# Kernel tuning notes

Hardware: AMD Instinct MI355X
Metric: run time of the kernel (lower is better)

## Reference

```python
import jax, jax.numpy as jnp
import numpy as np

# 1x1 Conv2d == channel contraction
def _conv(x, w):
    return jnp.einsum('bctn,oc->botn', x, w)

# BatchNorm2d in eval mode; p rows = (gamma, beta, running_mean, running_var)
def _bn(x, p, eps=1e-5):
    g, b, m, v = p
    s = g * jax.lax.rsqrt(v + eps)
    return x * s[None, :, None, None] + (b - m * s)[None, :, None, None]


def _forward(x, pos_2d, w_pos, b_pos, w_expand, bn_expand, w1, bn1, w2, bn2,
             w_ag, bn_ag, w_ag_s, b_ag_s, w_att, bn_att, w_att_s, b_att_s, W):
    B, T, J, Cp, N = x.shape
    C = J * Cp
    # rearrange 'b t j c n -> b (j c) t n'
    f = x.transpose(0, 2, 3, 1, 4).reshape(B, C, T, N)
    # pairwise expansion: h[b,:,t,i,j] = concat(f[b,:,t,i], f[b,:,t,j])  -> (B,2C,T,N*N)
    x1 = jnp.broadcast_to(f[:, :, :, :, None], (B, C, T, N, N))
    x2 = jnp.broadcast_to(f[:, :, :, None, :], (B, C, T, N, N))
    h = jnp.concatenate([x1, x2], axis=1).reshape(B, 2 * C, T, N * N)
    # relative 2D position embedding (first 2 coord channels)
    p = pos_2d[:, :, :, :2, :].transpose(0, 2, 3, 1, 4).reshape(B, 2 * J, T, N)
    rel = (p[:, :, :, :, None] - p[:, :, :, None, :]).reshape(B, 2 * J, T, N * N)
    pos_emb = _conv(rel, w_pos) + b_pos[None, :, None, None]
    # VAL trunk (dropout = identity in eval)
    h = jax.nn.relu(_bn(_conv(h, w_expand), bn_expand)) + pos_emb
    res = h
    h = jax.nn.relu(_bn(_conv(h, w1), bn1))
    h = jax.nn.relu(_bn(_conv(h, w2), bn2))
    h = res + h
    ag = _conv(jax.nn.relu(_bn(_conv(h, w_ag), bn_ag)), w_ag_s) + b_ag_s[None, :, None, None]
    ag = ag.reshape(B, -1, T, N, N)          # (B,Co,T,N,N)
    att = _conv(jax.nn.relu(_bn(_conv(h, w_att), bn_att)), w_att_s) + b_att_s[None, :, None, None]
    att = att.reshape(B, 1, T, N, N)
    # self / transfer terms, broadcast over receiver axis i
    f_self = jnp.einsum('bctn,cd->bdtn', f, W[0])[:, :, :, None, :]  # (B,Co,T,1,N)
    f_tran = jnp.einsum('bctn,cd->bdtn', f, W[1])[:, :, :, None, :] * ag
    E = jnp.eye(N, dtype=f.dtype)[None, None, None]                  # (1,1,1,N,N)
    f_conv = E * f_self + (1.0 - E) * f_tran
    att = jax.nn.softmax(att, axis=-1)
    f_fuse = jnp.sum(f_conv * att, axis=-1) + f                      # (B,Co,T,N)
    return f_fuse.reshape(B, J, Cp, T, N).transpose(0, 3, 1, 2, 4)   # (B,T,J,Cp,N)


def setup_inputs() -> dict:
    key = jax.random.key(0)
    ks = iter(jax.random.split(key, 64))
    B, T, J, Cp, N = 8, 128, 17, 32, 4
    C = J * Cp            # 544
    Cin = 2 * C           # 1088 (VAL in_channels)
    Co = C                # 544 (out_channels)

    def w(shape, s=0.03):
        return jax.random.normal(next(ks), shape, jnp.float32) * s

    def bn(c):
        return jnp.stack([
            1.0 + 0.1 * jax.random.normal(next(ks), (c,), jnp.float32),
            0.1 * jax.random.normal(next(ks), (c,), jnp.float32),
            0.1 * jax.random.normal(next(ks), (c,), jnp.float32),
            0.5 + jax.random.uniform(next(ks), (c,), jnp.float32),
        ])

    return dict(
        x=jax.random.normal(next(ks), (B, T, J, Cp, N), jnp.float32),
        pos_2d=jax.random.normal(next(ks), (B, T, J, 2, N), jnp.float32),
        w_pos=w((Cin, 2 * J)), b_pos=w((Cin,)),
        w_expand=w((Cin, Cin)), bn_expand=bn(Cin),
        w1=w((Cin, Cin)), bn1=bn(Cin),
        w2=w((Cin, Cin)), bn2=bn(Cin),
        w_ag=w((Cin, Cin)), bn_ag=bn(Cin),
        w_ag_s=w((Co, Cin)), b_ag_s=w((Co,)),
        w_att=w((Cin, Cin)), bn_att=bn(Cin),
        w_att_s=w((1, Cin)), b_att_s=w((1,)),
        W=w((2, Co, Co), 0.05),
    )


def reference(x, pos_2d, w_pos, b_pos, w_expand, bn_expand, w1, bn1, w2, bn2,
              w_ag, bn_ag, w_ag_s, b_ag_s, w_att, bn_att, w_att_s, b_att_s, W):
    return _forward(x, pos_2d, w_pos, b_pos, w_expand, bn_expand, w1, bn1, w2, bn2,
                    w_ag, bn_ag, w_ag_s, b_ag_s, w_att, bn_att, w_att_s, b_att_s, W)
```

## Files before the change

kernel.cpp:

```cpp
#include <hip/hip_runtime.h>

typedef unsigned short u16;
typedef unsigned int   u32;
typedef __attribute__((ext_vector_type(4))) float f32x4;
typedef __attribute__((ext_vector_type(8))) short short8;

#define DI static __device__ __forceinline__

DI u16 f2bf(float x){ union{float f;u32 u;}v; v.f=x; u32 r=v.u + 0x7fffu + ((v.u>>16)&1u); return (u16)(r>>16); }
DI float bf2f(u16 h){ union{u32 u;float f;}v; v.u=((u32)h)<<16; return v.f; }

DI void gl_lds16(const u16* g, u16* l){
  __builtin_amdgcn_global_load_lds((const __attribute__((address_space(1))) void*)g,
                                   (__attribute__((address_space(3))) void*)l, 16, 0, 0);
}


__global__ void k_bnprep(const float* __restrict__ bnE, const float* __restrict__ bn1,
                         const float* __restrict__ bn2, const float* __restrict__ bnA,
                         const float* __restrict__ bnT, float* __restrict__ out){
  int i = blockIdx.x*256 + threadIdx.x;
  if(i >= 5*1088) return;
  int w = i/1088, c = i - w*1088;
  const float* b = (w==0)?bnE:(w==1)?bn1:(w==2)?bn2:(w==3)?bnA:bnT;
  float g=b[c], be=b[1088+c], mu=b[2176+c], va=b[3264+c];
  float s = g / sqrtf(va + 1e-5f);
  out[w*2176 + c] = s;
  out[w*2176 + 1088 + c] = be - mu*s;
}

__global__ void k_zero(float* p, int n){ int i = blockIdx.x*256+threadIdx.x; if(i<n) p[i]=0.f; }

__global__ void k_pack_f(const float* __restrict__ x, float* __restrict__ fmat,
                         u16* __restrict__ fhi, u16* __restrict__ flo){
  int bt = blockIdx.x;
  const float* xr = x + (size_t)bt*2176;
  for(int t=threadIdx.x; t<2176; t+=256){
    int c = t>>2, n = t&3;
    float v = xr[t];
    size_t o = (size_t)(bt*4+n)*544 + c;
    fmat[o] = v;
    u16 h = f2bf(v); fhi[o]=h; flo[o]=f2bf(v - bf2f(h));
  }
}

__global__ void k_pack_w(const float* __restrict__ src, int off1, int off2, int O1,
                         int rs, int cs, int O, int K,
                         u16* __restrict__ dhi, u16* __restrict__ dlo){
  int o = blockIdx.y;
  int k = blockIdx.x*256 + threadIdx.x;
  if(k >= K) return;
  float v = 0.f;
  if(o < O){
    size_t idx = (o<O1) ? (size_t)off1 + (size_t)o*rs + (size_t)k*cs
                        : (size_t)off2 + (size_t)(o-O1)*rs + (size_t)k*cs;
    v = src[idx];
  }
  size_t d = (size_t)o*K + k;
  u16 h=f2bf(v); dhi[d]=h; dlo[d]=f2bf(v - bf2f(h));
}

__global__ void k_q(const float* __restrict__ pos, const float* __restrict__ w_pos,
                    float* __restrict__ q){
  int m = blockIdx.x; int bt = m>>2, n = m&3;
  __shared__ float pr[34];
  if(threadIdx.x<34){ int j = threadIdx.x>>1, d = threadIdx.x&1;
    pr[threadIdx.x] = pos[(size_t)bt*136 + j*8 + d*4 + n]; }
  __syncthreads();
  for(int o=threadIdx.x;o<1088;o+=256){
    const float* wr = w_pos + (size_t)o*34;
    float s = 0.f;
    #pragma unroll
    for(int k=0;k<34;k++) s += pr[k]*wr[k];
    q[(size_t)m*1088 + o] = s;
  }
}

__global__ void k_expand(const float* __restrict__ uv, const float* __restrict__ q,
                         const float* __restrict__ bn, const float* __restrict__ b_pos,
                         u16* __restrict__ hh, u16* __restrict__ hl){
  __shared__ float su[4][1088], sv[4][1088], sq[4][1088];
  int bt = blockIdx.x;
  for(int t=threadIdx.x; t<4*1088; t+=256){
    int r = t/1088, o = t - r*1088;
    su[r][o] = uv[(size_t)(bt*4+r)*2176 + o];
    sv[r][o] = uv[(size_t)(bt*4+r)*2176 + 1088 + o];
    sq[r][o] = q[(size_t)(bt*4+r)*1088 + o];
  }
  __syncthreads();
  for(int t=threadIdx.x; t<16*1088; t+=256){
    int ij = t/1088, o = t - ij*1088; int i = ij>>2, j = ij&3;
    float xv = bn[o]*(su[i][o]+sv[j][o]) + bn[1088+o];
    xv = fmaxf(xv,0.f) + sq[i][o]-sq[j][o]+b_pos[o];
    size_t idx = (size_t)(bt*16+ij)*1088 + o;
    u16 h=f2bf(xv); hh[idx]=h; hl[idx]=f2bf(xv-bf2f(h));
  }
}

template<int EPI>
__global__ __launch_bounds__(256,2)
void k_gemm(const u16* __restrict__ Ahi, const u16* __restrict__ Alo,
            const u16* __restrict__ Bhi, const u16* __restrict__ Blo,
            int K, int Nout, int ldo,
            float* __restrict__ out_f, u16* __restrict__ out_hi, u16* __restrict__ out_lo,
            const float* __restrict__ sv, const float* __restrict__ tv,
            const u16* __restrict__ res_hi, const u16* __restrict__ res_lo,
            const float* __restrict__ bias,
            const float* __restrict__ wred, float* __restrict__ red_out)
{
  __shared__ u16 Ah[2][4096], Al[2][4096], Bh[2][4096], Bl[2][4096];
  __shared__ float red[128];
  const int tid = threadIdx.x, lane = tid&63, wave = tid>>6;
  const int wm = wave>>1, wn = wave&1;

  const int gx = gridDim.x, gy = gridDim.y;
  const int flat = blockIdx.y*gx + blockIdx.x;
  const int chunk = (gx*gy) >> 3;
  const int p = (flat & 7)*chunk + (flat >> 3);
  const int bx = p/gy, by = p - bx*gy;
  const int m0 = bx*128, n0 = by*128;
  if(EPI==4 && tid<128) red[tid]=0.f;

  auto stage = [&](int buf, int kt){
    const int k0 = kt*32;
    #pragma unroll
    for(int c=0;c<2;c++){
      int s   = (wave*2+c)*64 + lane;
      int row = s>>2;
      int kg  = (s&3) ^ ((row>>1)&3);
      size_t ga = (size_t)(m0+row)*K + k0 + kg*8;
      size_t gb = (size_t)(n0+row)*K + k0 + kg*8;
      int lo = (wave*2+c)*512;
      gl_lds16(Ahi+ga, &Ah[buf][lo]);
      gl_lds16(Alo+ga, &Al[buf][lo]);
      gl_lds16(Bhi+gb, &Bh[buf][lo]);
      gl_lds16(Blo+gb, &Bl[buf][lo]);
    }
  };

  f32x4 acc[4][4];
  #pragma unroll
  for(int i=0;i<4;i++)
    #pragma unroll
    for(int j=0;j<4;j++){ acc[i][j][0]=0.f; acc[i][j][1]=0.f; acc[i][j][2]=0.f; acc[i][j][3]=0.f; }

  const int NT = K>>5;
  stage(0,0);
  stage(1,1);
  asm volatile("s_waitcnt vmcnt(8)" ::: "memory");
  __builtin_amdgcn_sched_barrier(0);
  __builtin_amdgcn_s_barrier();

  const int swz = ((lane>>4) ^ (((lane&15)>>1)&3))<<3;
  const int iA = ((wm*64 + (lane&15))<<5) + swz;
  const int iB = ((wn*64 + (lane&15))<<5) + swz;

  for(int kt=0; kt<NT; ++kt){
    const int buf = kt&1;
    short8 ah[4],al[4],bh[4],bl[4];
    #pragma unroll
    for(int i=0;i<4;i++){
      ah[i] = *(const short8*)&Ah[buf][iA + i*512];
      al[i] = *(const short8*)&Al[buf][iA + i*512];
      bh[i] = *(const short8*)&Bh[buf][iB + i*512];
      bl[i] = *(const short8*)&Bl[buf][iB + i*512];
    }
    asm volatile("s_waitcnt lgkmcnt(0)" ::: "memory");
    __builtin_amdgcn_sched_barrier(0);
    __builtin_amdgcn_s_barrier();
    int kt2 = kt+2; if(kt2 > NT-1) kt2 = NT-1;
    stage(buf, kt2);
    __builtin_amdgcn_s_setprio(1);
    #pragma unroll
    for(int mi=0;mi<4;mi++)
      #pragma unroll
      for(int ni=0;ni<4;ni++)
        acc[mi][ni] = __builtin_amdgcn_mfma_f32_16x16x32_bf16(ah[mi],bh[ni],acc[mi][ni],0,0,0);
    #pragma unroll
    for(int mi=0;mi<4;mi++)
      #pragma unroll
      for(int ni=0;ni<4;ni++)
        acc[mi][ni] = __builtin_amdgcn_mfma_f32_16x16x32_bf16(al[mi],bh[ni],acc[mi][ni],0,0,0);
    #pragma unroll
    for(int mi=0;mi<4;mi++)
      #pragma unroll
      for(int ni=0;ni<4;ni++)
        acc[mi][ni] = __builtin_amdgcn_mfma_f32_16x16x32_bf16(ah[mi],bl[ni],acc[mi][ni],0,0,0);
    __builtin_amdgcn_s_setprio(0);
    asm volatile("s_waitcnt vmcnt(8)" ::: "memory");
    __builtin_amdgcn_sched_barrier(0);
    __builtin_amdgcn_s_barrier();
  }

  const int r0 = m0 + wm*64 + ((lane>>4)<<2);
  const int c0 = n0 + wn*64 + (lane&15);

  if constexpr (EPI==0){
    #pragma unroll
    for(int mi=0;mi<4;mi++)
      #pragma unroll
      for(int ni=0;ni<4;ni++){
        int col = c0 + ni*16;
        if(col < Nout){
          #pragma unroll
          for(int r=0;r<4;r++)
            out_f[(size_t)(r0+mi*16+r)*ldo + col] = acc[mi][ni][r];
        }
      }
  } else if constexpr (EPI==1 || EPI==2){
    #pragma unroll
    for(int mi=0;mi<4;mi++)
      #pragma unroll
      for(int ni=0;ni<4;ni++){
        int col = c0 + ni*16;
        if(col < Nout){
          float sc = sv[col], tc = tv[col];
          #pragma unroll
          for(int r=0;r<4;r++){
            float y = fmaxf(acc[mi][ni][r]*sc + tc, 0.f);
            size_t idx = (size_t)(r0+mi*16+r)*ldo + col;
            if(EPI==2) y += bf2f(res_hi[idx]) + bf2f(res_lo[idx]);
            u16 h = f2bf(y); out_hi[idx]=h; out_lo[idx]=f2bf(y - bf2f(h));
          }
        }
      }
  } else if constexpr (EPI==3){
    #pragma unroll
    for(int mi=0;mi<4;mi++)
      #pragma unroll
      for(int ni=0;ni<4;ni++){
        int col = c0 + ni*16;
        if(col < Nout){
          float bc = bias[col];
          #pragma unroll
          for(int r=0;r<4;r++)
            out_f[(size_t)(r0+mi*16+r)*ldo + col] = acc[mi][ni][r] + bc;
        }
      }
  } else {
    float rs4[4][4];
    #pragma unroll
    for(int mi=0;mi<4;mi++)
      #pragma unroll
      for(int r=0;r<4;r++) rs4[mi][r]=0.f;
    #pragma unroll
    for(int mi=0;mi<4;mi++)
      #pragma unroll
      for(int ni=0;ni<4;ni++){
        int col = c0 + ni*16;
        if(col < Nout){
          float sc = sv[col], tc = tv[col], wc = wred[col];
          #pragma unroll
          for(int r=0;r<4;r++)
            rs4[mi][r] += fmaxf(acc[mi][ni][r]*sc + tc, 0.f)*wc;
        }
      }
    #pragma unroll
    for(int off=1; off<16; off<<=1)
      #pragma unroll
      for(int mi=0;mi<4;mi++)
        #pragma unroll
        for(int r=0;r<4;r++)
          rs4[mi][r] += __shfl_xor(rs4[mi][r], off, 64);
    if((lane&15)==0){
      #pragma unroll
      for(int mi=0;mi<4;mi++)
        #pragma unroll
        for(int r=0;r<4;r++)
          atomicAdd(&red[wm*64 + mi*16 + ((lane>>4)<<2) + r], rs4[mi][r]);
    }
    __syncthreads();
    if(tid<128) atomicAdd(&red_out[m0+tid], red[tid]);
  }
}

__global__ void k_fuse(const float* __restrict__ logits, const float* __restrict__ ag,
                       const float* __restrict__ fsft, const float* __restrict__ fmat,
                       float* __restrict__ out){
  int bt = blockIdx.x;
  float a[4][4];
  #pragma unroll
  for(int i=0;i<4;i++){
    float l0=logits[bt*16+i*4+0], l1=logits[bt*16+i*4+1],
          l2=logits[bt*16+i*4+2], l3=logits[bt*16+i*4+3];
    float mx = fmaxf(fmaxf(l0,l1),fmaxf(l2,l3));
    float e0=__expf(l0-mx), e1=__expf(l1-mx), e2=__expf(l2-mx), e3=__expf(l3-mx);
    float inv = 1.f/(e0+e1+e2+e3);
    a[i][0]=e0*inv; a[i][1]=e1*inv; a[i][2]=e2*inv; a[i][3]=e3*inv;
  }
  for(int d=threadIdx.x; d<544; d+=256){
    float fsv[4], ftv[4], fv[4];
    #pragma unroll
    for(int j=0;j<4;j++){
      fsv[j] = fsft[(size_t)(bt*4+j)*1088 + d];
      ftv[j] = fsft[(size_t)(bt*4+j)*1088 + 544 + d];
      fv[j]  = fmat[(size_t)(bt*4+j)*544 + d];
    }
    float o4[4];
    #pragma unroll
    for(int i=0;i<4;i++){
      float s = fv[i];
      #pragma unroll
      for(int j=0;j<4;j++){
        float fc = (j==i) ? fsv[j] : ftv[j]*ag[(size_t)(bt*16+i*4+j)*544 + d];
        s += a[i][j]*fc;
      }
      o4[i]=s;
    }
    *(float4*)(out + ((size_t)bt*544 + d)*4) = make_float4(o4[0],o4[1],o4[2],o4[3]);
  }
}

extern "C" void kernel_launch(void* const* d_in, const int* in_sizes, int n_in,
                              void* d_out, int out_size, void* d_ws, size_t ws_size,
                              hipStream_t stream){
  (void)in_sizes; (void)n_in; (void)out_size; (void)ws_size;
  const float* x      = (const float*)d_in[0];
  const float* pos2d  = (const float*)d_in[1];
  const float* w_pos  = (const float*)d_in[2];
  const float* b_pos  = (const float*)d_in[3];
  const float* w_exp  = (const float*)d_in[4];
  const float* bnE    = (const float*)d_in[5];
  const float* w1     = (const float*)d_in[6];
  const float* bn1    = (const float*)d_in[7];
  const float* w2     = (const float*)d_in[8];
  const float* bn2    = (const float*)d_in[9];
  const float* w_ag   = (const float*)d_in[10];
  const float* bnA    = (const float*)d_in[11];
  const float* w_ag_s = (const float*)d_in[12];
  const float* b_ag_s = (const float*)d_in[13];
  const float* w_att  = (const float*)d_in[14];
  const float* bnT    = (const float*)d_in[15];
  const float* w_att_s= (const float*)d_in[16];
  const float* Wm     = (const float*)d_in[18];
  float* out = (float*)d_out;

  char* ws = (char*)d_ws;
  size_t off = 0;
  auto alloc = [&](size_t b)->char*{ char* p = ws+off; off += (b+255)&~(size_t)255; return p; };

  float* fmat  = (float*)alloc(8912896);
  u16*   fhi   = (u16*)  alloc(4456448);
  u16*   flo   = (u16*)  alloc(4456448);
  float* bnbuf = (float*)alloc(43520);
  u16*   wuv   = (u16*)  alloc(5013504);
  u16*   w1p   = (u16*)  alloc(5013504);
  u16*   w2p   = (u16*)  alloc(5013504);
  u16*   wagp  = (u16*)  alloc(5013504);
  u16*   watp  = (u16*)  alloc(5013504);
  u16*   wagsp = (u16*)  alloc(2785280);
  u16*   wWp   = (u16*)  alloc(2506752);
  float* logits= (float*)alloc(65536);
  char*  X0    = alloc(71303168);
  char*  X1    = alloc(71303168);
  char*  X2    = alloc(71303168);

  u16* h0h=(u16*)X0;            u16* h0l=(u16*)(X0+35651584);
  u16* a1h=(u16*)X0;            u16* a1l=(u16*)(X0+35651584);
  float* qb =(float*)X1;
  u16* r1h=(u16*)X1;            u16* r1l=(u16*)(X1+35651584);
  float* agb =(float*)X1;       float* fsft=(float*)(X1+35651584);
  float* uvb =(float*)X2;
  u16* h2h=(u16*)X2;            u16* h2l=(u16*)(X2+35651584);

  k_bnprep<<<22,256,0,stream>>>(bnE,bn1,bn2,bnA,bnT,bnbuf);
  k_zero  <<<64,256,0,stream>>>(logits,16384);
  k_pack_f<<<1024,256,0,stream>>>(x, fmat, fhi, flo);
  k_pack_w<<<dim3(3,2304),256,0,stream>>>(w_exp, 0,544,1088, 1088,1, 2176,544, wuv, wuv+2304*544);
  k_pack_w<<<dim3(5,1152),256,0,stream>>>(w1,   0,0,1088, 1088,1, 1088,1088, w1p, w1p+1152*1088);
  k_pack_w<<<dim3(5,1152),256,0,stream>>>(w2,   0,0,1088, 1088,1, 1088,1088, w2p, w2p+1152*1088);
  k_pack_w<<<dim3(5,1152),256,0,stream>>>(w_ag, 0,0,1088, 1088,1, 1088,1088, wagp, wagp+1152*1088);
  k_pack_w<<<dim3(5,1152),256,0,stream>>>(w_att,0,0,1088, 1088,1, 1088,1088, watp, watp+1152*1088);
  k_pack_w<<<dim3(5, 640),256,0,stream>>>(w_ag_s,0,0, 544, 1088,1,  544,1088, wagsp, wagsp+640*1088);
  k_pack_w<<<dim3(3,1152),256,0,stream>>>(Wm, 0,544*544,544, 1,544, 1088,544, wWp, wWp+1152*544);
  k_q<<<4096,256,0,stream>>>(pos2d, w_pos, qb);

  k_gemm<0><<<dim3(32,18),256,0,stream>>>(fhi,flo, wuv,wuv+2304*544, 544, 2176, 2176,
      uvb, nullptr,nullptr, nullptr,nullptr, nullptr,nullptr, nullptr, nullptr,nullptr);
  k_expand<<<1024,256,0,stream>>>(uvb, qb, bnbuf, b_pos, h0h, h0l);
  k_gemm<1><<<dim3(128,9),256,0,stream>>>(h0h,h0l, w1p,w1p+1152*1088, 1088, 1088, 1088,
      nullptr, r1h,r1l, bnbuf+2176, bnbuf+2176+1088, nullptr,nullptr, nullptr, nullptr,nullptr);
  k_gemm<2><<<dim3(128,9),256,0,stream>>>(r1h,r1l, w2p,w2p+1152*1088, 1088, 1088, 1088,
      nullptr, h2h,h2l, bnbuf+2*2176, bnbuf+2*2176+1088, h0h,h0l, nullptr, nullptr,nullptr);
  k_gemm<1><<<dim3(128,9),256,0,stream>>>(h2h,h2l, wagp,wagp+1152*1088, 1088, 1088, 1088,
      nullptr, a1h,a1l, bnbuf+3*2176, bnbuf+3*2176+1088, nullptr,nullptr, nullptr, nullptr,nullptr);
  k_gemm<3><<<dim3(128,5),256,0,stream>>>(a1h,a1l, wagsp,wagsp+640*1088, 1088, 544, 544,
      agb, nullptr,nullptr, nullptr,nullptr, nullptr,nullptr, b_ag_s, nullptr,nullptr);
  k_gemm<4><<<dim3(128,9),256,0,stream>>>(h2h,h2l, watp,watp+1152*1088, 1088, 1088, 1088,
      nullptr, nullptr,nullptr, bnbuf+4*2176, bnbuf+4*2176+1088, nullptr,nullptr, nullptr,
      w_att_s, logits);
  k_gemm<0><<<dim3(32,9),256,0,stream>>>(fhi,flo, wWp,wWp+1152*544, 544, 1088, 1088,
      fsft, nullptr,nullptr, nullptr,nullptr, nullptr,nullptr, nullptr, nullptr,nullptr);
  k_fuse<<<1024,256,0,stream>>>(logits, agb, fsft, fmat, out);
}
```

Baseline: 935.7 us.

## Double-buffer LDS fragment registers to overlap LDS reads with MFMA in GEMM

Restructures the GEMM main loop so the LDS-to-register fragment loads for the next k-tile are issued before the MFMA block of the current tile, using two register fragment sets swapped across a 2x unrolled loop. This is meant to hide LDS read latency behind matrix-core work. The cost is a doubled fragment register footprint, which could lower occupancy or cause spills. The global-load wait also changes from vmcnt(8) to vmcnt(0), which may expose more global-load latency.

```diff
diff --git a/kernel.cpp b/kernel.cpp
--- a/kernel.cpp
+++ b/kernel.cpp
@@ -121,6 +121,8 @@
   const int m0 = bx*128, n0 = by*128;
   if(EPI==4 && tid<128) red[tid]=0.f;
 
+  const int NT = K>>5;
+
   auto stage = [&](int buf, int kt){
     const int k0 = kt*32;
     #pragma unroll
@@ -138,59 +140,77 @@
     }
   };
 
+  const int swz = ((lane>>4) ^ (((lane&15)>>1)&3))<<3;
+  const int iA = ((wm*64 + (lane&15))<<5) + swz;
+  const int iB = ((wn*64 + (lane&15))<<5) + swz;
+
+  struct Frags { short8 ah[4], al[4], bh[4], bl[4]; };
+  Frags fx, fy;
+
+  auto ldfrags = [&](Frags& f, int buf){
+    #pragma unroll
+    for(int i=0;i<4;i++){
+      f.ah[i] = *(const short8*)&Ah[buf][iA + i*512];
+      f.al[i] = *(const short8*)&Al[buf][iA + i*512];
+      f.bh[i] = *(const short8*)&Bh[buf][iB + i*512];
+      f.bl[i] = *(const short8*)&Bl[buf][iB + i*512];
+    }
+  };
+
   f32x4 acc[4][4];
   #pragma unroll
   for(int i=0;i<4;i++)
     #pragma unroll
     for(int j=0;j<4;j++){ acc[i][j][0]=0.f; acc[i][j][1]=0.f; acc[i][j][2]=0.f; acc[i][j][3]=0.f; }
 
-  const int NT = K>>5;
+  auto mfma_all = [&](Frags& f){
+    #pragma unroll
+    for(int mi=0;mi<4;mi++)
+      #pragma unroll
+      for(int ni=0;ni<4;ni++)
+        acc[mi][ni] = __builtin_amdgcn_mfma_f32_16x16x32_bf16(f.ah[mi],f.bh[ni],acc[mi][ni],0,0,0);
+    #pragma unroll
+    for(int mi=0;mi<4;mi++)
+      #pragma unroll
+      for(int ni=0;ni<4;ni++)
+        acc[mi][ni] = __builtin_amdgcn_mfma_f32_16x16x32_bf16(f.al[mi],f.bh[ni],acc[mi][ni],0,0,0);
+    #pragma unroll
+    for(int mi=0;mi<4;mi++)
+      #pragma unroll
+      for(int ni=0;ni<4;ni++)
+        acc[mi][ni] = __builtin_amdgcn_mfma_f32_16x16x32_bf16(f.ah[mi],f.bl[ni],acc[mi][ni],0,0,0);
+  };
+
+  auto body = [&](Frags& cur, Frags& nxt, int kt){
+    asm volatile("s_waitcnt vmcnt(0)" ::: "memory");
+    __builtin_amdgcn_sched_barrier(0);
+    __builtin_amdgcn_s_barrier();
+    if(kt+1 < NT) ldfrags(nxt, (kt+1)&1);
+    int kt2 = kt+2; if(kt2 > NT-1) kt2 = NT-1;
+    stage(kt&1, kt2);
+    __builtin_amdgcn_sched_barrier(0);
+    __builtin_amdgcn_s_setprio(1);
+    mfma_all(cur);
+    __builtin_amdgcn_s_setprio(0);
+    __builtin_amdgcn_sched_barrier(0);
+    asm volatile("s_waitcnt lgkmcnt(0)" ::: "memory");
+    __builtin_amdgcn_sched_barrier(0);
+  };
+
   stage(0,0);
   stage(1,1);
   asm volatile("s_waitcnt vmcnt(8)" ::: "memory");
   __builtin_amdgcn_sched_barrier(0);
   __builtin_amdgcn_s_barrier();
-
-  const int swz = ((lane>>4) ^ (((lane&15)>>1)&3))<<3;
-  const int iA = ((wm*64 + (lane&15))<<5) + swz;
-  const int iB = ((wn*64 + (lane&15))<<5) + swz;
-
-  for(int kt=0; kt<NT; ++kt){
-    const int buf = kt&1;
-    short8 ah[4],al[4],bh[4],bl[4];
-    #pragma unroll
-    for(int i=0;i<4;i++){
-      ah[i] = *(const short8*)&Ah[buf][iA + i*512];
-      al[i] = *(const short8*)&Al[buf][iA + i*512];
-      bh[i] = *(const short8*)&Bh[buf][iB + i*512];
-      bl[i] = *(const short8*)&Bl[buf][iB + i*512];
-    }
-    asm volatile("s_waitcnt lgkmcnt(0)" ::: "memory");
-    __builtin_amdgcn_sched_barrier(0);
-    __builtin_amdgcn_s_barrier();
-    int kt2 = kt+2; if(kt2 > NT-1) kt2 = NT-1;
-    stage(buf, kt2);
-    __builtin_amdgcn_s_setprio(1);
-    #pragma unroll
-    for(int mi=0;mi<4;mi++)
-      #pragma unroll
-      for(int ni=0;ni<4;ni++)
-        acc[mi][ni] = __builtin_amdgcn_mfma_f32_16x16x32_bf16(ah[mi],bh[ni],acc[mi][ni],0,0,0);
-    #pragma unroll
-    for(int mi=0;mi<4;mi++)
-      #pragma unroll
-      for(int ni=0;ni<4;ni++)
-        acc[mi][ni] = __builtin_amdgcn_mfma_f32_16x16x32_bf16(al[mi],bh[ni],acc[mi][ni],0,0,0);
-    #pragma unroll
-    for(int mi=0;mi<4;mi++)
-      #pragma unroll
-      for(int ni=0;ni<4;ni++)
-        acc[mi][ni] = __builtin_amdgcn_mfma_f32_16x16x32_bf16(ah[mi],bl[ni],acc[mi][ni],0,0,0);
-    __builtin_amdgcn_s_setprio(0);
-    asm volatile("s_waitcnt vmcnt(8)" ::: "memory");
-    __builtin_amdgcn_sched_barrier(0);
-    __builtin_amdgcn_s_barrier();
-  }
+  ldfrags(fx, 0);
+  asm volatile("s_waitcnt lgkmcnt(0)" ::: "memory");
+  __builtin_amdgcn_sched_barrier(0);
+
+  for(int kt=0; kt+1<NT; kt+=2){
+    body(fx, fy, kt);
+    body(fy, fx, kt+1);
+  }
+  if(NT & 1) body(fx, fy, NT-1);
 
   const int r0 = m0 + wm*64 + ((lane>>4)<<2);
   const int c0 = n0 + wn*64 + (lane&15);
```

Measured after the change: 954.1 us. About the same (+2.0%).

## Use 256x128 tiles with 8 waves and triple-buffered LDS pipeline in GEMM

Applied to the files above, without the earlier changes.

The GEMM kernel moves to 512 threads per block with a 256-row M tile, so each B tile is shared by twice as many rows. It replaces the double buffer with a three-stage LDS ring and interleaves the split LDS fragment reads with the three bf16 MFMA passes. This is meant to raise data reuse and hide global-to-LDS latency with one barrier per k-step. LDS use grows to roughly 150KB per block, and the launch_bounds(512,2) target may not be reachable, which would cut occupancy. The first GEMM grid is also changed from 18 to 17 column blocks.

```diff
diff --git a/kernel.cpp b/kernel.cpp
--- a/kernel.cpp
+++ b/kernel.cpp
@@ -98,7 +98,7 @@
 }
 
 template<int EPI>
-__global__ __launch_bounds__(256,2)
+__global__ __launch_bounds__(512,2)
 void k_gemm(const u16* __restrict__ Ahi, const u16* __restrict__ Alo,
             const u16* __restrict__ Bhi, const u16* __restrict__ Blo,
             int K, int Nout, int ldo,
@@ -108,8 +108,8 @@
             const float* __restrict__ bias,
             const float* __restrict__ wred, float* __restrict__ red_out)
 {
-  __shared__ u16 Ah[2][4096], Al[2][4096], Bh[2][4096], Bl[2][4096];
-  __shared__ float red[128];
+  __shared__ u16 Ah[3][8192], Al[3][8192], Bh[3][4096], Bl[3][4096];
+  __shared__ float red[256];
   const int tid = threadIdx.x, lane = tid&63, wave = tid>>6;
   const int wm = wave>>1, wn = wave&1;
 
@@ -118,10 +118,12 @@
   const int chunk = (gx*gy) >> 3;
   const int p = (flat & 7)*chunk + (flat >> 3);
   const int bx = p/gy, by = p - bx*gy;
-  const int m0 = bx*128, n0 = by*128;
-  if(EPI==4 && tid<128) red[tid]=0.f;
-
-  auto stage = [&](int buf, int kt){
+  const int m0 = bx*256, n0 = by*128;
+  if(EPI==4 && tid<256) red[tid]=0.f;
+
+  const int NT = K>>5;
+
+  auto stage = [&](int sb, int kt){
     const int k0 = kt*32;
     #pragma unroll
     for(int c=0;c<2;c++){
@@ -129,14 +131,24 @@
       int row = s>>2;
       int kg  = (s&3) ^ ((row>>1)&3);
       size_t ga = (size_t)(m0+row)*K + k0 + kg*8;
+      int lo = (wave*2+c)*512;
+      gl_lds16(Ahi+ga, &Ah[sb][lo]);
+      gl_lds16(Alo+ga, &Al[sb][lo]);
+    }
+    {
+      int s   = wave*64 + lane;
+      int row = s>>2;
+      int kg  = (s&3) ^ ((row>>1)&3);
       size_t gb = (size_t)(n0+row)*K + k0 + kg*8;
-      int lo = (wave*2+c)*512;
-      gl_lds16(Ahi+ga, &Ah[buf][lo]);
-      gl_lds16(Alo+ga, &Al[buf][lo]);
-      gl_lds16(Bhi+gb, &Bh[buf][lo]);
-      gl_lds16(Blo+gb, &Bl[buf][lo]);
+      int lo = wave*512;
+      gl_lds16(Bhi+gb, &Bh[sb][lo]);
+      gl_lds16(Blo+gb, &Bl[sb][lo]);
     }
   };
+
+  const int swz = ((lane>>4) ^ (((lane&15)>>1)&3))<<3;
+  const int iA = ((wm*64 + (lane&15))<<5) + swz;
+  const int iB = ((wn*64 + (lane&15))<<5) + swz;
 
   f32x4 acc[4][4];
   #pragma unroll
@@ -144,52 +156,56 @@
     #pragma unroll
     for(int j=0;j<4;j++){ acc[i][j][0]=0.f; acc[i][j][1]=0.f; acc[i][j][2]=0.f; acc[i][j][3]=0.f; }
 
-  const int NT = K>>5;
   stage(0,0);
   stage(1,1);
-  asm volatile("s_waitcnt vmcnt(8)" ::: "memory");
-  __builtin_amdgcn_sched_barrier(0);
-  __builtin_amdgcn_s_barrier();
-
-  const int swz = ((lane>>4) ^ (((lane&15)>>1)&3))<<3;
-  const int iA = ((wm*64 + (lane&15))<<5) + swz;
-  const int iB = ((wn*64 + (lane&15))<<5) + swz;
-
+
+  short8 ah[4],al[4],bh[4],bl[4];
   for(int kt=0; kt<NT; ++kt){
-    const int buf = kt&1;
-    short8 ah[4],al[4],bh[4],bl[4];
-    #pragma unroll
-    for(int i=0;i<4;i++){
-      ah[i] = *(const short8*)&Ah[buf][iA + i*512];
-      al[i] = *(const short8*)&Al[buf][iA + i*512];
-      bh[i] = *(const short8*)&Bh[buf][iB + i*512];
-      bl[i] = *(const short8*)&Bl[buf][iB + i*512];
-    }
-    asm volatile("s_waitcnt lgkmcnt(0)" ::: "memory");
+    const int rb = kt%3;
+    if(kt==NT-1) asm volatile("s_waitcnt vmcnt(0)" ::: "memory");
+    else         asm volatile("s_waitcnt vmcnt(6)" ::: "memory");
     __builtin_amdgcn_sched_barrier(0);
     __builtin_amdgcn_s_barrier();
-    int kt2 = kt+2; if(kt2 > NT-1) kt2 = NT-1;
-    stage(buf, kt2);
+    #pragma unroll
+    for(int i=0;i<4;i++) ah[i] = *(const short8*)&Ah[rb][iA + i*512];
+    #pragma unroll
+    for(int i=0;i<4;i++) bh[i] = *(const short8*)&Bh[rb][iB + i*512];
+    __builtin_amdgcn_sched_barrier(0);
+    #pragma unroll
+    for(int i=0;i<4;i++) al[i] = *(const short8*)&Al[rb][iA + i*512];
+    asm volatile("s_waitcnt lgkmcnt(4)" ::: "memory");
+    __builtin_amdgcn_sched_barrier(0);
     __builtin_amdgcn_s_setprio(1);
     #pragma unroll
     for(int mi=0;mi<4;mi++)
       #pragma unroll
       for(int ni=0;ni<4;ni++)
         acc[mi][ni] = __builtin_amdgcn_mfma_f32_16x16x32_bf16(ah[mi],bh[ni],acc[mi][ni],0,0,0);
+    __builtin_amdgcn_s_setprio(0);
+    __builtin_amdgcn_sched_barrier(0);
+    #pragma unroll
+    for(int i=0;i<4;i++) bl[i] = *(const short8*)&Bl[rb][iB + i*512];
+    asm volatile("s_waitcnt lgkmcnt(4)" ::: "memory");
+    __builtin_amdgcn_sched_barrier(0);
+    __builtin_amdgcn_s_setprio(1);
     #pragma unroll
     for(int mi=0;mi<4;mi++)
       #pragma unroll
       for(int ni=0;ni<4;ni++)
         acc[mi][ni] = __builtin_amdgcn_mfma_f32_16x16x32_bf16(al[mi],bh[ni],acc[mi][ni],0,0,0);
+    __builtin_amdgcn_s_setprio(0);
+    __builtin_amdgcn_sched_barrier(0);
+    if(kt+2 < NT) stage((kt+2)%3, kt+2);
+    asm volatile("s_waitcnt lgkmcnt(0)" ::: "memory");
+    __builtin_amdgcn_sched_barrier(0);
+    __builtin_amdgcn_s_setprio(1);
     #pragma unroll
     for(int mi=0;mi<4;mi++)
       #pragma unroll
       for(int ni=0;ni<4;ni++)
         acc[mi][ni] = __builtin_amdgcn_mfma_f32_16x16x32_bf16(ah[mi],bl[ni],acc[mi][ni],0,0,0);
     __builtin_amdgcn_s_setprio(0);
-    asm volatile("s_waitcnt vmcnt(8)" ::: "memory");
-    __builtin_amdgcn_sched_barrier(0);
-    __builtin_amdgcn_s_barrier();
+    __builtin_amdgcn_sched_barrier(0);
   }
 
   const int r0 = m0 + wm*64 + ((lane>>4)<<2);
@@ -270,7 +286,7 @@
           atomicAdd(&red[wm*64 + mi*16 + ((lane>>4)<<2) + r], rs4[mi][r]);
     }
     __syncthreads();
-    if(tid<128) atomicAdd(&red_out[m0+tid], red[tid]);
+    if(tid<256) atomicAdd(&red_out[m0+tid], red[tid]);
   }
 }
 
@@ -375,21 +391,21 @@
   k_pack_w<<<dim3(3,1152),256,0,stream>>>(Wm, 0,544*544,544, 1,544, 1088,544, wWp, wWp+1152*544);
   k_q<<<4096,256,0,stream>>>(pos2d, w_pos, qb);
 
-  k_gemm<0><<<dim3(32,18),256,0,stream>>>(fhi,flo, wuv,wuv+2304*544, 544, 2176, 2176,
+  k_gemm<0><<<dim3(16,17),512,0,stream>>>(fhi,flo, wuv,wuv+2304*544, 544, 2176, 2176,
       uvb, nullptr,nullptr, nullptr,nullptr, nullptr,nullptr, nullptr, nullptr,nullptr);
   k_expand<<<1024,256,0,stream>>>(uvb, qb, bnbuf, b_pos, h0h, h0l);
-  k_gemm<1><<<dim3(128,9),256,0,stream>>>(h0h,h0l, w1p,w1p+1152*1088, 1088, 1088, 1088,
+  k_gemm<1><<<dim3(64,9),512,0,stream>>>(h0h,h0l, w1p,w1p+1152*1088, 1088, 1088, 1088,
       nullptr, r1h,r1l, bnbuf+2176, bnbuf+2176+1088, nullptr,nullptr, nullptr, nullptr,nullptr);
-  k_gemm<2><<<dim3(128,9),256,0,stream>>>(r1h,r1l, w2p,w2p+1152*1088, 1088, 1088, 1088,
+  k_gemm<2><<<dim3(64,9),512,0,stream>>>(r1h,r1l, w2p,w2p+1152*1088, 1088, 1088, 1088,
       nullptr, h2h,h2l, bnbuf+2*2176, bnbuf+2*2176+1088, h0h,h0l, nullptr, nullptr,nullptr);
-  k_gemm<1><<<dim3(128,9),256,0,stream>>>(h2h,h2l, wagp,wagp+1152*1088, 1088, 1088, 1088,
+  k_gemm<1><<<dim3(64,9),512,0,stream>>>(h2h,h2l, wagp,wagp+1152*1088, 1088, 1088, 1088,
       nullptr, a1h,a1l, bnbuf+3*2176, bnbuf+3*2176+1088, nullptr,nullptr, nullptr, nullptr,nullptr);
-  k_gemm<3><<<dim3(128,5),256,0,stream>>>(a1h,a1l, wagsp,wagsp+640*1088, 1088, 544, 544,
+  k_gemm<3><<<dim3(64,5),512,0,stream>>>(a1h,a1l, wagsp,wagsp+640*1088, 1088, 544, 544,
       agb, nullptr,nullptr, nullptr,nullptr, nullptr,nullptr, b_ag_s, nullptr,nullptr);
-  k_gemm<4><<<dim3(128,9),256,0,stream>>>(h2h,h2l, watp,watp+1152*1088, 1088, 1088, 1088,
+  k_gemm<4><<<dim3(64,9),512,0,stream>>>(h2h,h2l, watp,watp+1152*1088, 1088, 1088, 1088,
       nullptr, nullptr,nullptr, bnbuf+4*2176, bnbuf+4*2176+1088, nullptr,nullptr, nullptr,
       w_att_s, logits);
-  k_gemm<0><<<dim3(32,9),256,0,stream>>>(fhi,flo, wWp,wWp+1152*544, 544, 1088, 1088,
+  k_gemm<0><<<dim3(16,9),512,0,stream>>>(fhi,flo, wWp,wWp+1152*544, 544, 1088, 1088,
       fsft, nullptr,nullptr, nullptr,nullptr, nullptr,nullptr, nullptr, nullptr,nullptr);
   k_fuse<<<1024,256,0,stream>>>(logits, agb, fsft, fmat, out);
 }
```

Result: slower. 978.4 us (+4.6%).
